# Performance work log

Measured on AMD Instinct MI355X. Metric: run time of the kernel, lower is better.

The kernel has to match this reference:

```python
import jax, jax.numpy as jnp
import numpy as np

N = 100000   # nodes
E = 800000   # edges
D = 64       # feature dim (input=hidden=output)
EPS = 1e-5   # BatchNorm eps


def setup_inputs() -> dict:
    key = jax.random.key(0)
    ks = jax.random.split(key, 24)
    s = 1.0 / np.sqrt(D)
    inp = {
        "x": jax.random.normal(ks[0], (N, D), jnp.float32),
        "edge_index": jax.random.randint(ks[1], (2, E), 0, N, jnp.int64),
        # GCNConv weights (x @ W + b after normalized aggregation)
        "W1": jax.random.normal(ks[2], (D, D), jnp.float32) * s,
        "b1": jax.random.normal(ks[3], (D,), jnp.float32) * 0.01,
        "W2": jax.random.normal(ks[4], (D, D), jnp.float32) * s,
        "b2": jax.random.normal(ks[5], (D,), jnp.float32) * 0.01,
        "W3": jax.random.normal(ks[6], (D, D), jnp.float32) * s,
        "b3": jax.random.normal(ks[7], (D,), jnp.float32) * 0.01,
        # BatchNorm1d (inference: running stats)
        "bn1_g": jax.random.uniform(ks[8], (D,), jnp.float32, 0.5, 1.5),
        "bn1_b": jax.random.normal(ks[9], (D,), jnp.float32) * 0.1,
        "bn1_m": jax.random.normal(ks[10], (D,), jnp.float32) * 0.1,
        "bn1_v": jax.random.uniform(ks[11], (D,), jnp.float32, 0.5, 1.5),
        "bn2_g": jax.random.uniform(ks[12], (D,), jnp.float32, 0.5, 1.5),
        "bn2_b": jax.random.normal(ks[13], (D,), jnp.float32) * 0.1,
        "bn2_m": jax.random.normal(ks[14], (D,), jnp.float32) * 0.1,
        "bn2_v": jax.random.uniform(ks[15], (D,), jnp.float32, 0.5, 1.5),
        # predictor MLP: Linear -> tanh -> (dropout=id) -> Linear
        "pW1": jax.random.normal(ks[16], (D, D), jnp.float32) * s,
        "pb1": jax.random.normal(ks[17], (D,), jnp.float32) * 0.01,
        "pW2": jax.random.normal(ks[18], (D, D), jnp.float32) * s,
        "pb2": jax.random.normal(ks[19], (D,), jnp.float32) * 0.01,
    }
    return inp


def _gcn_norm(edge_index):
    # add self loops, compute sym-normalized edge coefficients (PyG GCNConv)
    loop = jnp.arange(N, dtype=edge_index.dtype)
    src = jnp.concatenate([edge_index[0], loop])
    dst = jnp.concatenate([edge_index[1], loop])
    deg = jax.ops.segment_sum(jnp.ones(src.shape[0], jnp.float32), dst, num_segments=N)
    dis = jax.lax.rsqrt(deg)  # deg >= 1 due to self loops
    norm = dis[src] * dis[dst]
    return src, dst, norm


def _gcn_layer(x, src, dst, norm, W, b):
    h = x @ W                              # [N, D] small GEMM
    msg = h[src] * norm[:, None]           # [E+N, D] gather (memory bound)
    return jax.ops.segment_sum(msg, dst, num_segments=N) + b  # scatter-add


def _bn(x, g, b, m, v):
    return (x - m) * (g * jax.lax.rsqrt(v + EPS)) + b


def reference(x, edge_index, W1, b1, W2, b2, W3, b3,
              bn1_g, bn1_b, bn1_m, bn1_v, bn2_g, bn2_b, bn2_m, bn2_v,
              pW1, pb1, pW2, pb2):
    src, dst, norm = _gcn_norm(edge_index)
    h = _gcn_layer(x, src, dst, norm, W1, b1)
    h = jax.nn.relu(_bn(h, bn1_g, bn1_b, bn1_m, bn1_v))   # dropout = id (eval)
    h = _gcn_layer(h, src, dst, norm, W2, b2)
    h = jax.nn.relu(_bn(h, bn2_g, bn2_b, bn2_m, bn2_v))
    h = _gcn_layer(h, src, dst, norm, W3, b3)
    out = jnp.tanh(h @ pW1 + pb1) @ pW2 + pb2              # predictor MLP
    return out
```

## Files before the change

### kernel.cpp

```cpp
#include <hip/hip_runtime.h>
#include <hip/hip_fp16.h>

#define N_NODES 100000
#define N_EDGES 800000
#define DIM 64
#define BN_EPS 1e-5f
#define LDX 68
#define EDGE_CAP 1600000


__global__ __launch_bounds__(256) void k_count(const int* __restrict__ dst,
                                               int* __restrict__ deg) {
    int e = blockIdx.x * blockDim.x + threadIdx.x;
    if (e < N_EDGES) atomicAdd(&deg[dst[e]], 1);
}

__global__ __launch_bounds__(256) void k_scan(const int* __restrict__ deg,
                                              int* __restrict__ row_off,
                                              int* __restrict__ cursor,
                                              float* __restrict__ dinv,
                                              int* __restrict__ gcount) {
    __shared__ int sdata[256];
    __shared__ int sbase;
    int tid = threadIdx.x;
    int base = blockIdx.x * 1024 + tid * 4;
    int4 d = make_int4(0, 0, 0, 0);
    int4 v = make_int4(0, 0, 0, 0);
    if (base < N_NODES) {
        d = *(const int4*)(deg + base);
        v.x = (d.x + 7) & ~7;
        v.y = (d.y + 7) & ~7;
        v.z = (d.z + 7) & ~7;
        v.w = (d.w + 7) & ~7;
    }
    int tsum = v.x + v.y + v.z + v.w;
    sdata[tid] = tsum;
    __syncthreads();
    for (int off = 1; off < 256; off <<= 1) {
        int t = (tid >= off) ? sdata[tid - off] : 0;
        __syncthreads();
        sdata[tid] += t;
        __syncthreads();
    }
    if (tid == 255) sbase = atomicAdd(gcount, sdata[255]);
    __syncthreads();
    if (base >= N_NODES) return;
    int excl = sdata[tid] - tsum + sbase;
    int4 o;
    o.x = excl;
    o.y = o.x + v.x;
    o.z = o.y + v.y;
    o.w = o.z + v.z;
    *(int4*)(row_off + base) = o;
    *(int4*)(cursor + base) = o;
    float4 di;
    di.x = rsqrtf((float)(d.x + 1));
    di.y = rsqrtf((float)(d.y + 1));
    di.z = rsqrtf((float)(d.z + 1));
    di.w = rsqrtf((float)(d.w + 1));
    *(float4*)(dinv + base) = di;
}

__global__ __launch_bounds__(256) void k_build(const int* __restrict__ ei,
                                               const float* __restrict__ dinv,
                                               int* __restrict__ cursor,
                                               int2* __restrict__ edges) {
    int e = blockIdx.x * blockDim.x + threadIdx.x;
    if (e >= N_EDGES) return;
    int s = ei[e];
    int d = ei[N_EDGES + e];
    int pos = atomicAdd(&cursor[d], 1);
    edges[pos] = make_int2(s, __float_as_int(dinv[s] * dinv[d]));
}

__global__ __launch_bounds__(256) void k_tohalf(const float* __restrict__ x,
                                                __half* __restrict__ xh) {
    int idx = blockIdx.x * blockDim.x + threadIdx.x;
    float4 v = ((const float4*)x)[idx];
    unsigned int u0 = __half_as_ushort(__float2half(v.x));
    unsigned int u1 = __half_as_ushort(__float2half(v.y));
    unsigned int u2 = __half_as_ushort(__float2half(v.z));
    unsigned int u3 = __half_as_ushort(__float2half(v.w));
    ((uint2*)xh)[idx] = make_uint2(u0 | (u1 << 16), u2 | (u3 << 16));
}

__global__ __launch_bounds__(256) void k_fuse_w3(const float* __restrict__ W3,
                                                 const float* __restrict__ b3,
                                                 const float* __restrict__ pW1,
                                                 const float* __restrict__ pb1,
                                                 float* __restrict__ W3p,
                                                 float* __restrict__ b3p) {
    int tid = threadIdx.x;
    int c = tid & 63;
    int kbase = (tid >> 6) * 16;
    for (int k = kbase; k < kbase + 16; ++k) {
        float acc = 0.f;
#pragma unroll 8
        for (int j = 0; j < 64; ++j)
            acc = fmaf(W3[k * 64 + j], pW1[j * 64 + c], acc);
        W3p[k * 64 + c] = acc;
    }
    if (tid < 64) {
        float acc = pb1[c];
#pragma unroll 8
        for (int j = 0; j < 64; ++j)
            acc = fmaf(b3[j], pW1[j * 64 + c], acc);
        b3p[c] = acc;
    }
}

__global__ __launch_bounds__(256) void k_aggregate(const __half* __restrict__ xin,
                                                   const int* __restrict__ row_off,
                                                   const int* __restrict__ deg,
                                                   const int2* __restrict__ edges,
                                                   const float* __restrict__ dinv,
                                                   float* __restrict__ out) {
    int lane = threadIdx.x & 63;
    int node = blockIdx.x * 4 + (threadIdx.x >> 6);
    float di = dinv[node];
    float acc = __half2float(xin[(size_t)node * DIM + lane]) * (di * di);
    int beg = __builtin_amdgcn_readfirstlane(row_off[node]);
    int lenp = (__builtin_amdgcn_readfirstlane(deg[node]) + 7) & ~7;
    int end = beg + lenp;
    for (int k = beg; k < end; k += 8) {
        int2 e0 = edges[k + 0];
        int2 e1 = edges[k + 1];
        int2 e2 = edges[k + 2];
        int2 e3 = edges[k + 3];
        int2 e4 = edges[k + 4];
        int2 e5 = edges[k + 5];
        int2 e6 = edges[k + 6];
        int2 e7 = edges[k + 7];
        float v0 = __half2float(xin[(size_t)e0.x * DIM + lane]);
        float v1 = __half2float(xin[(size_t)e1.x * DIM + lane]);
        float v2 = __half2float(xin[(size_t)e2.x * DIM + lane]);
        float v3 = __half2float(xin[(size_t)e3.x * DIM + lane]);
        float v4 = __half2float(xin[(size_t)e4.x * DIM + lane]);
        float v5 = __half2float(xin[(size_t)e5.x * DIM + lane]);
        float v6 = __half2float(xin[(size_t)e6.x * DIM + lane]);
        float v7 = __half2float(xin[(size_t)e7.x * DIM + lane]);
        acc = fmaf(__int_as_float(e0.y), v0, acc);
        acc = fmaf(__int_as_float(e1.y), v1, acc);
        acc = fmaf(__int_as_float(e2.y), v2, acc);
        acc = fmaf(__int_as_float(e3.y), v3, acc);
        acc = fmaf(__int_as_float(e4.y), v4, acc);
        acc = fmaf(__int_as_float(e5.y), v5, acc);
        acc = fmaf(__int_as_float(e6.y), v6, acc);
        acc = fmaf(__int_as_float(e7.y), v7, acc);
    }
    out[(size_t)node * DIM + lane] = acc;
}

#define GEMM_STEP(SX, SW)                                                      \
    {                                                                          \
        float4 a0 = *(const float4*)&SX[(r0 + 0) * LDX + k4 * 4];              \
        float4 a1 = *(const float4*)&SX[(r0 + 1) * LDX + k4 * 4];              \
        float4 a2 = *(const float4*)&SX[(r0 + 2) * LDX + k4 * 4];              \
        float4 a3 = *(const float4*)&SX[(r0 + 3) * LDX + k4 * 4];              \
        float4 b0 = *(const float4*)&SW[(k4 * 4 + 0) * 64 + c0];               \
        float4 b1 = *(const float4*)&SW[(k4 * 4 + 1) * 64 + c0];               \
        float4 b2 = *(const float4*)&SW[(k4 * 4 + 2) * 64 + c0];               \
        float4 b3 = *(const float4*)&SW[(k4 * 4 + 3) * 64 + c0];               \
        const float* ap[4] = {&a0.x, &a1.x, &a2.x, &a3.x};                     \
        _Pragma("unroll") for (int i = 0; i < 4; ++i) {                        \
            float x0 = ap[i][0], x1 = ap[i][1], x2 = ap[i][2], x3 = ap[i][3];  \
            acc[i][0] = fmaf(x0, b0.x, acc[i][0]);                             \
            acc[i][1] = fmaf(x0, b0.y, acc[i][1]);                             \
            acc[i][2] = fmaf(x0, b0.z, acc[i][2]);                             \
            acc[i][3] = fmaf(x0, b0.w, acc[i][3]);                             \
            acc[i][0] = fmaf(x1, b1.x, acc[i][0]);                             \
            acc[i][1] = fmaf(x1, b1.y, acc[i][1]);                             \
            acc[i][2] = fmaf(x1, b1.z, acc[i][2]);                             \
            acc[i][3] = fmaf(x1, b1.w, acc[i][3]);                             \
            acc[i][0] = fmaf(x2, b2.x, acc[i][0]);                             \
            acc[i][1] = fmaf(x2, b2.y, acc[i][1]);                             \
            acc[i][2] = fmaf(x2, b2.z, acc[i][2]);                             \
            acc[i][3] = fmaf(x2, b2.w, acc[i][3]);                             \
            acc[i][0] = fmaf(x3, b3.x, acc[i][0]);                             \
            acc[i][1] = fmaf(x3, b3.y, acc[i][1]);                             \
            acc[i][2] = fmaf(x3, b3.z, acc[i][2]);                             \
            acc[i][3] = fmaf(x3, b3.w, acc[i][3]);                             \
        }                                                                      \
    }

__global__ __launch_bounds__(256) void k_gemm_bn_h(const float* __restrict__ xin,
                                                   const float* __restrict__ W,
                                                   const float* __restrict__ bias,
                                                   const float* __restrict__ bng,
                                                   const float* __restrict__ bnb,
                                                   const float* __restrict__ bnm,
                                                   const float* __restrict__ bnv,
                                                   __half* __restrict__ out) {
    __shared__ float sW[4096];
    __shared__ float sX[64 * LDX];
    int tid = threadIdx.x;
    int row0 = blockIdx.x * 64;

    for (int i = tid; i < 1024; i += 256)
        ((float4*)sW)[i] = ((const float4*)W)[i];
    {
        int r = tid >> 2;
        int q = tid & 3;
        int row = row0 + r;
        float4* dst = (float4*)(sX + r * LDX);
        if (row < N_NODES) {
            const float4* src = (const float4*)(xin + (size_t)row * DIM);
#pragma unroll
            for (int m = 0; m < 4; ++m) dst[q + m * 4] = src[q + m * 4];
        } else {
            float4 z = make_float4(0.f, 0.f, 0.f, 0.f);
#pragma unroll
            for (int m = 0; m < 4; ++m) dst[q + m * 4] = z;
        }
    }
    __syncthreads();

    int cq = tid & 15, rq = tid >> 4;
    int c0 = cq * 4, r0 = rq * 4;
    float acc[4][4];
#pragma unroll
    for (int i = 0; i < 4; ++i)
#pragma unroll
        for (int j = 0; j < 4; ++j) acc[i][j] = 0.f;

#pragma unroll 4
    for (int k4 = 0; k4 < 16; ++k4) GEMM_STEP(sX, sW)

    float4 bv = *(const float4*)&bias[c0];
    float4 g = *(const float4*)&bng[c0];
    float4 bb = *(const float4*)&bnb[c0];
    float4 m = *(const float4*)&bnm[c0];
    float4 vv = *(const float4*)&bnv[c0];
    float A0 = g.x * rsqrtf(vv.x + BN_EPS);
    float A1 = g.y * rsqrtf(vv.y + BN_EPS);
    float A2 = g.z * rsqrtf(vv.z + BN_EPS);
    float A3 = g.w * rsqrtf(vv.w + BN_EPS);
    float B0 = (bv.x - m.x) * A0 + bb.x;
    float B1 = (bv.y - m.y) * A1 + bb.y;
    float B2 = (bv.z - m.z) * A2 + bb.z;
    float B3 = (bv.w - m.w) * A3 + bb.w;
#pragma unroll
    for (int i = 0; i < 4; ++i) {
        int row = row0 + r0 + i;
        if (row >= N_NODES) break;
        unsigned int u0 = __half_as_ushort(__float2half(fmaxf(0.f, fmaf(acc[i][0], A0, B0))));
        unsigned int u1 = __half_as_ushort(__float2half(fmaxf(0.f, fmaf(acc[i][1], A1, B1))));
        unsigned int u2 = __half_as_ushort(__float2half(fmaxf(0.f, fmaf(acc[i][2], A2, B2))));
        unsigned int u3 = __half_as_ushort(__float2half(fmaxf(0.f, fmaf(acc[i][3], A3, B3))));
        *(uint2*)(out + (size_t)row * DIM + c0) = make_uint2(u0 | (u1 << 16), u2 | (u3 << 16));
    }
}

__global__ __launch_bounds__(256) void k_tail(const float* __restrict__ xin,
                                              const float* __restrict__ W3p,
                                              const float* __restrict__ b3p,
                                              const float* __restrict__ pW2,
                                              const float* __restrict__ pb2,
                                              float* __restrict__ out) {
    __shared__ float sW1[4096];
    __shared__ float sW2[4096];
    __shared__ float sX[64 * LDX];
    int tid = threadIdx.x;
    int row0 = blockIdx.x * 64;

    for (int i = tid; i < 1024; i += 256) {
        ((float4*)sW1)[i] = ((const float4*)W3p)[i];
        ((float4*)sW2)[i] = ((const float4*)pW2)[i];
    }
    {
        int r = tid >> 2;
        int q = tid & 3;
        int row = row0 + r;
        float4* dst = (float4*)(sX + r * LDX);
        if (row < N_NODES) {
            const float4* src = (const float4*)(xin + (size_t)row * DIM);
#pragma unroll
            for (int m = 0; m < 4; ++m) dst[q + m * 4] = src[q + m * 4];
        } else {
            float4 z = make_float4(0.f, 0.f, 0.f, 0.f);
#pragma unroll
            for (int m = 0; m < 4; ++m) dst[q + m * 4] = z;
        }
    }
    __syncthreads();

    int cq = tid & 15, rq = tid >> 4;
    int c0 = cq * 4, r0 = rq * 4;
    float acc[4][4];

#pragma unroll
    for (int i = 0; i < 4; ++i)
#pragma unroll
        for (int j = 0; j < 4; ++j) acc[i][j] = 0.f;
#pragma unroll 4
    for (int k4 = 0; k4 < 16; ++k4) GEMM_STEP(sX, sW1)
    __syncthreads();

    {
        float4 bv = *(const float4*)&b3p[c0];
#pragma unroll
        for (int i = 0; i < 4; ++i) {
            float4 h;
            h.x = tanhf(acc[i][0] + bv.x);
            h.y = tanhf(acc[i][1] + bv.y);
            h.z = tanhf(acc[i][2] + bv.z);
            h.w = tanhf(acc[i][3] + bv.w);
            *(float4*)&sX[(r0 + i) * LDX + c0] = h;
        }
    }
    __syncthreads();

#pragma unroll
    for (int i = 0; i < 4; ++i)
#pragma unroll
        for (int j = 0; j < 4; ++j) acc[i][j] = 0.f;
#pragma unroll 4
    for (int k4 = 0; k4 < 16; ++k4) GEMM_STEP(sX, sW2)

    float4 bv = *(const float4*)&pb2[c0];
#pragma unroll
    for (int i = 0; i < 4; ++i) {
        int row = row0 + r0 + i;
        if (row >= N_NODES) break;
        float4 o;
        o.x = acc[i][0] + bv.x;
        o.y = acc[i][1] + bv.y;
        o.z = acc[i][2] + bv.z;
        o.w = acc[i][3] + bv.w;
        *(float4*)(out + (size_t)row * DIM + c0) = o;
    }
}

extern "C" void kernel_launch(void* const* d_in, const int* in_sizes, int n_in,
                              void* d_out, int out_size, void* d_ws, size_t ws_size,
                              hipStream_t stream) {
    const float* x     = (const float*)d_in[0];
    const int*   ei    = (const int*)d_in[1];
    const float* W1    = (const float*)d_in[2];
    const float* b1    = (const float*)d_in[3];
    const float* W2    = (const float*)d_in[4];
    const float* b2    = (const float*)d_in[5];
    const float* W3    = (const float*)d_in[6];
    const float* b3    = (const float*)d_in[7];
    const float* bn1_g = (const float*)d_in[8];
    const float* bn1_b = (const float*)d_in[9];
    const float* bn1_m = (const float*)d_in[10];
    const float* bn1_v = (const float*)d_in[11];
    const float* bn2_g = (const float*)d_in[12];
    const float* bn2_b = (const float*)d_in[13];
    const float* bn2_m = (const float*)d_in[14];
    const float* bn2_v = (const float*)d_in[15];
    const float* pW1   = (const float*)d_in[16];
    const float* pb1   = (const float*)d_in[17];
    const float* pW2   = (const float*)d_in[18];
    const float* pb2   = (const float*)d_in[19];
    float* out = (float*)d_out;

    char* ws = (char*)d_ws;
    int*   deg      = (int*)ws;                      ws += 100352 * 4;
    int*   gcount   = (int*)ws;                      ws += 4 * 4;
    int*   row_off  = (int*)ws;                      ws += 100352 * 4;
    int*   cursor   = (int*)ws;                      ws += 100352 * 4;
    int2*  edges    = (int2*)ws;                     ws += (size_t)EDGE_CAP * 8;
    float* dinv     = (float*)ws;                    ws += 100352 * 4;
    float* W3p      = (float*)ws;                    ws += 4096 * 4;
    float* b3p      = (float*)ws;                    ws += 64 * 4;
    __half* xh      = (__half*)ws;                   ws += (size_t)N_NODES * DIM * 2;
    __half* hbuf    = (__half*)ws;                   ws += (size_t)N_NODES * DIM * 2;
    float* bufA     = (float*)ws;                    ws += (size_t)N_NODES * DIM * 4;

    const int blk = 256;
    int gE    = (N_EDGES + blk - 1) / blk;
    int gScan = 98;
    int gCvt  = N_NODES * 16 / blk;
    int gAgg  = N_NODES / 4;
    int gTile = (N_NODES + 63) / 64;

    hipMemsetAsync(deg, 0, (100352 + 4) * 4, stream);
    hipMemsetAsync(edges, 0, (size_t)EDGE_CAP * 8, stream);
    k_tohalf<<<gCvt, blk, 0, stream>>>(x, xh);
    k_count<<<gE, blk, 0, stream>>>(ei + N_EDGES, deg);
    k_scan<<<gScan, blk, 0, stream>>>(deg, row_off, cursor, dinv, gcount);
    k_build<<<gE, blk, 0, stream>>>(ei, dinv, cursor, edges);
    k_fuse_w3<<<1, blk, 0, stream>>>(W3, b3, pW1, pb1, W3p, b3p);

    k_aggregate<<<gAgg, blk, 0, stream>>>(xh, row_off, deg, edges, dinv, bufA);
    k_gemm_bn_h<<<gTile, blk, 0, stream>>>(bufA, W1, b1, bn1_g, bn1_b, bn1_m, bn1_v, hbuf);

    k_aggregate<<<gAgg, blk, 0, stream>>>(hbuf, row_off, deg, edges, dinv, bufA);
    k_gemm_bn_h<<<gTile, blk, 0, stream>>>(bufA, W2, b2, bn2_g, bn2_b, bn2_m, bn2_v, hbuf);

    k_aggregate<<<gAgg, blk, 0, stream>>>(hbuf, row_off, deg, edges, dinv, bufA);
    k_tail<<<gTile, blk, 0, stream>>>(bufA, W3p, b3p, pW2, pb2, out);
}
```

Baseline: 382.8 us.

## Fuse setup kernels and store aggregation output in fp16

Merges the fp32-to-fp16 conversion with degree counting, folds the W3/pW1 weight fusion into an extra block of the scan kernel, and collapses the two memsets into one. The aggregate kernel now writes fp16 instead of fp32, and the GEMM/tail kernels convert back to fp32 while staging into shared memory. This cuts launch count and halves the intermediate write/read traffic between aggregation and GEMM, at the cost of an extra fp16 rounding of pre-GEMM activations. The single memset relies on deg, gcount, row_off, cursor and edges being contiguous in the workspace, so it now also zeroes row_off and cursor.

```diff
diff --git a/kernel.cpp b/kernel.cpp
--- a/kernel.cpp
+++ b/kernel.cpp
@@ -8,21 +8,55 @@
 #define LDX 68
 #define EDGE_CAP 1600000
 
-
-__global__ __launch_bounds__(256) void k_count(const int* __restrict__ dst,
-                                               int* __restrict__ deg) {
-    int e = blockIdx.x * blockDim.x + threadIdx.x;
-    if (e < N_EDGES) atomicAdd(&deg[dst[e]], 1);
-}
-
-__global__ __launch_bounds__(256) void k_scan(const int* __restrict__ deg,
-                                              int* __restrict__ row_off,
-                                              int* __restrict__ cursor,
-                                              float* __restrict__ dinv,
-                                              int* __restrict__ gcount) {
+__global__ __launch_bounds__(256) void k_cvt_count(const float* __restrict__ x,
+                                                   __half* __restrict__ xh,
+                                                   const int* __restrict__ dst,
+                                                   int* __restrict__ deg) {
+    int idx = blockIdx.x * blockDim.x + threadIdx.x;
+    if (idx < 1600000) {
+        float4 v = ((const float4*)x)[idx];
+        unsigned int u0 = __half_as_ushort(__float2half(v.x));
+        unsigned int u1 = __half_as_ushort(__float2half(v.y));
+        unsigned int u2 = __half_as_ushort(__float2half(v.z));
+        unsigned int u3 = __half_as_ushort(__float2half(v.w));
+        ((uint2*)xh)[idx] = make_uint2(u0 | (u1 << 16), u2 | (u3 << 16));
+    }
+    if (idx < N_EDGES) atomicAdd(&deg[dst[idx]], 1);
+}
+
+__global__ __launch_bounds__(256) void k_scan_fuse(const int* __restrict__ deg,
+                                                   int* __restrict__ row_off,
+                                                   int* __restrict__ cursor,
+                                                   float* __restrict__ dinv,
+                                                   int* __restrict__ gcount,
+                                                   const float* __restrict__ W3,
+                                                   const float* __restrict__ b3,
+                                                   const float* __restrict__ pW1,
+                                                   const float* __restrict__ pb1,
+                                                   float* __restrict__ W3p,
+                                                   float* __restrict__ b3p) {
+    int tid = threadIdx.x;
+    if (blockIdx.x == 98) {
+        int c = tid & 63;
+        int kbase = (tid >> 6) * 16;
+        for (int k = kbase; k < kbase + 16; ++k) {
+            float acc = 0.f;
+#pragma unroll 8
+            for (int j = 0; j < 64; ++j)
+                acc = fmaf(W3[k * 64 + j], pW1[j * 64 + c], acc);
+            W3p[k * 64 + c] = acc;
+        }
+        if (tid < 64) {
+            float acc = pb1[c];
+#pragma unroll 8
+            for (int j = 0; j < 64; ++j)
+                acc = fmaf(b3[j], pW1[j * 64 + c], acc);
+            b3p[c] = acc;
+        }
+        return;
+    }
     __shared__ int sdata[256];
     __shared__ int sbase;
-    int tid = threadIdx.x;
     int base = blockIdx.x * 1024 + tid * 4;
     int4 d = make_int4(0, 0, 0, 0);
     int4 v = make_int4(0, 0, 0, 0);
@@ -73,48 +107,12 @@
     edges[pos] = make_int2(s, __float_as_int(dinv[s] * dinv[d]));
 }
 
-__global__ __launch_bounds__(256) void k_tohalf(const float* __restrict__ x,
-                                                __half* __restrict__ xh) {
-    int idx = blockIdx.x * blockDim.x + threadIdx.x;
-    float4 v = ((const float4*)x)[idx];
-    unsigned int u0 = __half_as_ushort(__float2half(v.x));
-    unsigned int u1 = __half_as_ushort(__float2half(v.y));
-    unsigned int u2 = __half_as_ushort(__float2half(v.z));
-    unsigned int u3 = __half_as_ushort(__float2half(v.w));
-    ((uint2*)xh)[idx] = make_uint2(u0 | (u1 << 16), u2 | (u3 << 16));
-}
-
-__global__ __launch_bounds__(256) void k_fuse_w3(const float* __restrict__ W3,
-                                                 const float* __restrict__ b3,
-                                                 const float* __restrict__ pW1,
-                                                 const float* __restrict__ pb1,
-                                                 float* __restrict__ W3p,
-                                                 float* __restrict__ b3p) {
-    int tid = threadIdx.x;
-    int c = tid & 63;
-    int kbase = (tid >> 6) * 16;
-    for (int k = kbase; k < kbase + 16; ++k) {
-        float acc = 0.f;
-#pragma unroll 8
-        for (int j = 0; j < 64; ++j)
-            acc = fmaf(W3[k * 64 + j], pW1[j * 64 + c], acc);
-        W3p[k * 64 + c] = acc;
-    }
-    if (tid < 64) {
-        float acc = pb1[c];
-#pragma unroll 8
-        for (int j = 0; j < 64; ++j)
-            acc = fmaf(b3[j], pW1[j * 64 + c], acc);
-        b3p[c] = acc;
-    }
-}
-
 __global__ __launch_bounds__(256) void k_aggregate(const __half* __restrict__ xin,
                                                    const int* __restrict__ row_off,
                                                    const int* __restrict__ deg,
                                                    const int2* __restrict__ edges,
                                                    const float* __restrict__ dinv,
-                                                   float* __restrict__ out) {
+                                                   __half* __restrict__ out) {
     int lane = threadIdx.x & 63;
     int node = blockIdx.x * 4 + (threadIdx.x >> 6);
     float di = dinv[node];
@@ -148,7 +146,7 @@
         acc = fmaf(__int_as_float(e6.y), v6, acc);
         acc = fmaf(__int_as_float(e7.y), v7, acc);
     }
-    out[(size_t)node * DIM + lane] = acc;
+    out[(size_t)node * DIM + lane] = __float2half(acc);
 }
 
 #define GEMM_STEP(SX, SW)                                                      \
@@ -183,7 +181,30 @@
         }                                                                      \
     }
 
-__global__ __launch_bounds__(256) void k_gemm_bn_h(const float* __restrict__ xin,
+#define STAGE_H2F(SRCPTR, SXPTR)                                               \
+    {                                                                          \
+        int r = tid >> 2;                                                      \
+        int q = tid & 3;                                                       \
+        int row = row0 + r;                                                    \
+        float4* dst = (float4*)(SXPTR + r * LDX);                              \
+        if (row < N_NODES) {                                                   \
+            const uint2* src = (const uint2*)(SRCPTR + (size_t)row * DIM);     \
+            _Pragma("unroll") for (int m = 0; m < 4; ++m) {                    \
+                uint2 u = src[q + m * 4];                                      \
+                float4 f;                                                      \
+                f.x = __half2float(__ushort_as_half((unsigned short)(u.x & 0xffff)));       \
+                f.y = __half2float(__ushort_as_half((unsigned short)(u.x >> 16)));          \
+                f.z = __half2float(__ushort_as_half((unsigned short)(u.y & 0xffff)));       \
+                f.w = __half2float(__ushort_as_half((unsigned short)(u.y >> 16)));          \
+                dst[q + m * 4] = f;                                            \
+            }                                                                  \
+        } else {                                                               \
+            float4 z = make_float4(0.f, 0.f, 0.f, 0.f);                        \
+            _Pragma("unroll") for (int m = 0; m < 4; ++m) dst[q + m * 4] = z;  \
+        }                                                                      \
+    }
+
+__global__ __launch_bounds__(256) void k_gemm_bn_h(const __half* __restrict__ xin,
                                                    const float* __restrict__ W,
                                                    const float* __restrict__ bias,
                                                    const float* __restrict__ bng,
@@ -198,21 +219,7 @@
 
     for (int i = tid; i < 1024; i += 256)
         ((float4*)sW)[i] = ((const float4*)W)[i];
-    {
-        int r = tid >> 2;
-        int q = tid & 3;
-        int row = row0 + r;
-        float4* dst = (float4*)(sX + r * LDX);
-        if (row < N_NODES) {
-            const float4* src = (const float4*)(xin + (size_t)row * DIM);
-#pragma unroll
-            for (int m = 0; m < 4; ++m) dst[q + m * 4] = src[q + m * 4];
-        } else {
-            float4 z = make_float4(0.f, 0.f, 0.f, 0.f);
-#pragma unroll
-            for (int m = 0; m < 4; ++m) dst[q + m * 4] = z;
-        }
-    }
+    STAGE_H2F(xin, sX)
     __syncthreads();
 
     int cq = tid & 15, rq = tid >> 4;
@@ -251,7 +258,7 @@
     }
 }
 
-__global__ __launch_bounds__(256) void k_tail(const float* __restrict__ xin,
+__global__ __launch_bounds__(256) void k_tail(const __half* __restrict__ xin,
                                               const float* __restrict__ W3p,
                                               const float* __restrict__ b3p,
                                               const float* __restrict__ pW2,
@@ -267,21 +274,7 @@
         ((float4*)sW1)[i] = ((const float4*)W3p)[i];
         ((float4*)sW2)[i] = ((const float4*)pW2)[i];
     }
-    {
-        int r = tid >> 2;
-        int q = tid & 3;
-        int row = row0 + r;
-        float4* dst = (float4*)(sX + r * LDX);
-        if (row < N_NODES) {
-            const float4* src = (const float4*)(xin + (size_t)row * DIM);
-#pragma unroll
-            for (int m = 0; m < 4; ++m) dst[q + m * 4] = src[q + m * 4];
-        } else {
-            float4 z = make_float4(0.f, 0.f, 0.f, 0.f);
-#pragma unroll
-            for (int m = 0; m < 4; ++m) dst[q + m * 4] = z;
-        }
-    }
+    STAGE_H2F(xin, sX)
     __syncthreads();
 
     int cq = tid & 15, rq = tid >> 4;
@@ -367,29 +360,27 @@
     float* b3p      = (float*)ws;                    ws += 64 * 4;
     __half* xh      = (__half*)ws;                   ws += (size_t)N_NODES * DIM * 2;
     __half* hbuf    = (__half*)ws;                   ws += (size_t)N_NODES * DIM * 2;
-    float* bufA     = (float*)ws;                    ws += (size_t)N_NODES * DIM * 4;
+    __half* abuf    = (__half*)ws;                   ws += (size_t)N_NODES * DIM * 2;
 
     const int blk = 256;
     int gE    = (N_EDGES + blk - 1) / blk;
-    int gScan = 98;
-    int gCvt  = N_NODES * 16 / blk;
+    int gCvt  = 6250;
     int gAgg  = N_NODES / 4;
     int gTile = (N_NODES + 63) / 64;
 
-    hipMemsetAsync(deg, 0, (100352 + 4) * 4, stream);
-    hipMemsetAsync(edges, 0, (size_t)EDGE_CAP * 8, stream);
-    k_tohalf<<<gCvt, blk, 0, stream>>>(x, xh);
-    k_count<<<gE, blk, 0, stream>>>(ei + N_EDGES, deg);
-    k_scan<<<gScan, blk, 0, stream>>>(deg, row_off, cursor, dinv, gcount);
+    size_t zbytes = (size_t)(100352 * 3 + 4) * 4 + (size_t)EDGE_CAP * 8;
+    hipMemsetAsync(deg, 0, zbytes, stream);
+    k_cvt_count<<<gCvt, blk, 0, stream>>>(x, xh, ei + N_EDGES, deg);
+    k_scan_fuse<<<99, blk, 0, stream>>>(deg, row_off, cursor, dinv, gcount,
+                                        W3, b3, pW1, pb1, W3p, b3p);
     k_build<<<gE, blk, 0, stream>>>(ei, dinv, cursor, edges);
-    k_fuse_w3<<<1, blk, 0, stream>>>(W3, b3, pW1, pb1, W3p, b3p);
-
-    k_aggregate<<<gAgg, blk, 0, stream>>>(xh, row_off, deg, edges, dinv, bufA);
-    k_gemm_bn_h<<<gTile, blk, 0, stream>>>(bufA, W1, b1, bn1_g, bn1_b, bn1_m, bn1_v, hbuf);
-
-    k_aggregate<<<gAgg, blk, 0, stream>>>(hbuf, row_off, deg, edges, dinv, bufA);
-    k_gemm_bn_h<<<gTile, blk, 0, stream>>>(bufA, W2, b2, bn2_g, bn2_b, bn2_m, bn2_v, hbuf);
-
-    k_aggregate<<<gAgg, blk, 0, stream>>>(hbuf, row_off, deg, edges, dinv, bufA);
-    k_tail<<<gTile, blk, 0, stream>>>(bufA, W3p, b3p, pW2, pb2, out);
-}
+
+    k_aggregate<<<gAgg, blk, 0, stream>>>(xh, row_off, deg, edges, dinv, abuf);
+    k_gemm_bn_h<<<gTile, blk, 0, stream>>>(abuf, W1, b1, bn1_g, bn1_b, bn1_m, bn1_v, hbuf);
+
+    k_aggregate<<<gAgg, blk, 0, stream>>>(hbuf, row_off, deg, edges, dinv, abuf);
+    k_gemm_bn_h<<<gTile, blk, 0, stream>>>(abuf, W2, b2, bn2_g, bn2_b, bn2_m, bn2_v, hbuf);
+
+    k_aggregate<<<gAgg, blk, 0, stream>>>(hbuf, row_off, deg, edges, dinv, abuf);
+    k_tail<<<gTile, blk, 0, stream>>>(abuf, W3p, b3p, pW2, pb2, out);
+}
```

After: 372.9 us. -2.6%, faster.
